# Kernel optimization log

Hardware: AMD Instinct MI355X
Metric: run time of the kernel (lower is better)

## Reference

```python
import jax, jax.numpy as jnp
import numpy as np

B, T, H, DK, DV, HID = 2, 2048, 6, 256, 256, 2048
EPS = 1e-5


def setup_inputs() -> dict:
    key = jax.random.key(0)
    ks = jax.random.split(key, 12)
    sd = 0.02
    hidden_ab = jax.random.normal(ks[0], (B, T, HID), jnp.float32)
    hidden_g = jax.random.normal(ks[1], (B, T, HID), jnp.float32)
    q = jax.random.normal(ks[2], (B, T, H, DK), jnp.float32)
    k = jax.random.normal(ks[3], (B, T, H, DK), jnp.float32)
    v = jax.random.normal(ks[4], (B, T, H, DV), jnp.float32)
    b_w = jax.random.normal(ks[5], (H, HID), jnp.float32) * sd
    a_w = jax.random.normal(ks[6], (H, HID), jnp.float32) * sd
    g_w = jax.random.normal(ks[7], (H, HID), jnp.float32) * sd
    A_log = jnp.log(jax.random.uniform(ks[8], (H,), jnp.float32, 1.0, 16.0))
    dt = jnp.exp(jax.random.uniform(ks[9], (H,), jnp.float32)
                 * (np.log(0.1) - np.log(0.001)) + np.log(0.001))
    dt = jnp.clip(dt, 1e-4)
    dt_bias = dt + jnp.log(-jnp.expm1(-dt))
    norm_w = jnp.ones((DV,), jnp.float32)
    o_w = jax.random.normal(ks[10], (H, DV, DK), jnp.float32) * sd
    return dict(hidden_ab=hidden_ab, hidden_g=hidden_g, q=q, k=k, v=v,
                b_w=b_w, a_w=a_w, A_log=A_log, dt_bias=dt_bias,
                g_w=g_w, norm_w=norm_w, o_w=o_w)


def _l2norm(x):
    return x * jax.lax.rsqrt(jnp.sum(x * x, axis=-1, keepdims=True) + 1e-6)


def _gated_delta_rule(q, k, v, g, beta):
    # q,k: [B,T,H,DK]; v: [B,T,H,DV]; g,beta: [B,T,H]
    q = _l2norm(q) * (DK ** -0.5)
    k = _l2norm(k)
    # time-major for scan
    qT = jnp.swapaxes(q, 0, 1)
    kT = jnp.swapaxes(k, 0, 1)
    vT = jnp.swapaxes(v, 0, 1)
    gT = jnp.swapaxes(g, 0, 1)
    bT = jnp.swapaxes(beta, 0, 1)

    def step(S, xs):
        qt, kt, vt, gt, bt = xs  # [B,H,*]
        S = S * jnp.exp(gt)[..., None, None]            # gated decay
        pred = jnp.einsum('bhk,bhkv->bhv', kt, S)        # current prediction
        delta = (vt - pred) * bt[..., None]              # beta-scaled error
        S = S + jnp.einsum('bhk,bhv->bhkv', kt, delta)   # delta-rule update
        ot = jnp.einsum('bhk,bhkv->bhv', qt, S)
        return S, ot

    S0 = jnp.zeros((B, H, DK, DV), q.dtype)
    _, oT = jax.lax.scan(step, S0, (qT, kT, vT, gT, bT))
    return jnp.swapaxes(oT, 0, 1)  # [B,T,H,DV]


def reference(hidden_ab, hidden_g, q, k, v, b_w, a_w, A_log, dt_bias, g_w, norm_w, o_w):
    beta = jax.nn.sigmoid(jnp.einsum('bth,nh->btn', hidden_ab, b_w))        # [B,T,H]
    g = -jnp.exp(A_log) * jax.nn.softplus(
        jnp.einsum('bth,nh->btn', hidden_ab, a_w) + dt_bias)                 # [B,T,H]
    o = _gated_delta_rule(q, k, v, g, beta)                                  # [B,T,H,DV]
    # FusedRMSNormSwishGate with per-head scalar gate
    gate = jnp.einsum('bth,nh->btn', hidden_g, g_w)                          # [B,T,H]
    o_n = o * jax.lax.rsqrt(jnp.mean(o * o, axis=-1, keepdims=True) + EPS) * norm_w
    o_n = o_n * (gate * jax.nn.sigmoid(gate))[..., None]
    # GroupLinear per head: head_v_dim -> head_dim
    out = jnp.einsum('bthv,hvd->bthd', o_n, o_w).reshape(B, T, H * DK)
    return out
```

## Files before the change

kernel.cpp:

```cpp
#include <hip/hip_runtime.h>
#include <hip/hip_bf16.h>
#include <math.h>

#define B_ 2
#define T_ 2048
#define H_ 6
#define DK_ 256
#define DV_ 256
#define HID_ 2048
#define C_ 64
#define NC_ 32

typedef __attribute__((ext_vector_type(8))) short short8;
typedef __attribute__((ext_vector_type(4))) float f32x4;

__device__ __forceinline__ unsigned rnebf(float f) {
  unsigned u = __float_as_uint(f);
  return (u + 0x7fffu + ((u >> 16) & 1u)) >> 16;
}
__device__ __forceinline__ unsigned pkbf(float lo, float hi) {
  return rnebf(lo) | (rnebf(hi) << 16);
}
__device__ __forceinline__ float bf2f(unsigned u16v) {
  return __uint_as_float((u16v & 0xffffu) << 16);
}
__device__ __forceinline__ short8 u4_to_s8(uint4 u) {
  union { uint4 u; short8 s; } c; c.u = u; return c.s;
}

__device__ __forceinline__ void gload_lds16(const void* g, void* l) {
  __builtin_amdgcn_global_load_lds(
      (const __attribute__((address_space(1))) unsigned int*)g,
      (__attribute__((address_space(3))) unsigned int*)l, 16, 0, 0);
}

__device__ __forceinline__ short8 buildB(uint2 Pe, uint2 Po, int lg, int c16) {
  const int src0 = ((2 * (lg & 1)) << 4) | c16;
  const int src1 = src0 + 16;
  int e0 = __shfl((int)Pe.x, src0), o0 = __shfl((int)Po.x, src0);
  int e1 = __shfl((int)Pe.y, src0), o1 = __shfl((int)Po.y, src0);
  int e2 = __shfl((int)Pe.x, src1), o2 = __shfl((int)Po.x, src1);
  int e3 = __shfl((int)Pe.y, src1), o3 = __shfl((int)Po.y, src1);
  const bool lo2 = (lg < 2);
  union { int i[4]; short8 s; } u;
  u.i[0] = lo2 ? e0 : o0;
  u.i[1] = lo2 ? e1 : o1;
  u.i[2] = lo2 ? e2 : o2;
  u.i[3] = lo2 ? e3 : o3;
  return u.s;
}

__global__ __launch_bounds__(256) void gdn_proj_kernel(
    const float* __restrict__ hab, const float* __restrict__ hg,
    const float* __restrict__ b_w, const float* __restrict__ a_w,
    const float* __restrict__ g_w, const float* __restrict__ A_log,
    const float* __restrict__ dt_bias,
    float* __restrict__ beta_o, float* __restrict__ g_o,
    float* __restrict__ sgate_o) {
  const int bt = blockIdx.x;
  const int tid = threadIdx.x;
  const int lane = tid & 63;
  const int wid = tid >> 6;

  const float* h1 = hab + (size_t)bt * HID_ + tid * 8;
  const float* h2 = hg + (size_t)bt * HID_ + tid * 8;
  const float4 xa = *(const float4*)(h1);
  const float4 xb = *(const float4*)(h1 + 4);
  const float4 ya = *(const float4*)(h2);
  const float4 yb = *(const float4*)(h2 + 4);

  float part[18];
#pragma unroll
  for (int n = 0; n < 6; ++n) {
    const float* wp = b_w + n * HID_ + tid * 8;
    const float4 w0 = *(const float4*)(wp);
    const float4 w1 = *(const float4*)(wp + 4);
    part[n] = xa.x * w0.x + xa.y * w0.y + xa.z * w0.z + xa.w * w0.w +
              xb.x * w1.x + xb.y * w1.y + xb.z * w1.z + xb.w * w1.w;
  }
#pragma unroll
  for (int n = 0; n < 6; ++n) {
    const float* wp = a_w + n * HID_ + tid * 8;
    const float4 w0 = *(const float4*)(wp);
    const float4 w1 = *(const float4*)(wp + 4);
    part[6 + n] = xa.x * w0.x + xa.y * w0.y + xa.z * w0.z + xa.w * w0.w +
                  xb.x * w1.x + xb.y * w1.y + xb.z * w1.z + xb.w * w1.w;
  }
#pragma unroll
  for (int n = 0; n < 6; ++n) {
    const float* wp = g_w + n * HID_ + tid * 8;
    const float4 w0 = *(const float4*)(wp);
    const float4 w1 = *(const float4*)(wp + 4);
    part[12 + n] = ya.x * w0.x + ya.y * w0.y + ya.z * w0.z + ya.w * w0.w +
                   yb.x * w1.x + yb.y * w1.y + yb.z * w1.z + yb.w * w1.w;
  }

  __shared__ float red[18][4];
#pragma unroll
  for (int i = 0; i < 18; ++i) {
    float x = part[i];
    x += __shfl_xor(x, 1);
    x += __shfl_xor(x, 2);
    x += __shfl_xor(x, 4);
    x += __shfl_xor(x, 8);
    x += __shfl_xor(x, 16);
    x += __shfl_xor(x, 32);
    if (lane == 0) red[i][wid] = x;
  }
  __syncthreads();

  if (tid < 18) {
    const float s = red[tid][0] + red[tid][1] + red[tid][2] + red[tid][3];
    if (tid < 6) {
      beta_o[(size_t)bt * H_ + tid] = 1.f / (1.f + __expf(-s));
    } else if (tid < 12) {
      const int n = tid - 6;
      const float x = s + dt_bias[n];
      const float sp = (x > 20.f) ? x : log1pf(__expf(x));
      g_o[(size_t)bt * H_ + n] = -__expf(A_log[n]) * sp;
    } else {
      const int n = tid - 12;
      sgate_o[(size_t)bt * H_ + n] = s / (1.f + __expf(-s));
    }
  }
}

__global__ __launch_bounds__(256) void gdn_cum_kernel(
    const float* __restrict__ g, float* __restrict__ Gc,
    float* __restrict__ lam) {
  const int bh = blockIdx.x;
  const int b = bh / H_, h = bh - b * H_;
  const int w = threadIdx.x >> 6, l = threadIdx.x & 63;
  for (int it = 0; it < 8; ++it) {
    const int nc = it * 4 + w;
    const int tg = nc * C_ + l;
    const size_t srow = ((size_t)b * T_ + tg) * H_ + h;
    float val = g[srow];
#pragma unroll
    for (int ofs = 1; ofs < 64; ofs <<= 1) {
      const float o = __shfl_up(val, ofs);
      if (l >= ofs) val += o;
    }
    Gc[(bh * NC_ + nc) * C_ + l] = val;
    if (l == 63) lam[bh * NC_ + nc] = __expf(val);
  }
}

__global__ __launch_bounds__(256) void gdn_prep_mfma_kernel(
    const float* __restrict__ q, const float* __restrict__ k,
    const float* __restrict__ beta, const float* __restrict__ Gc,
    ushort* __restrict__ wWp, ushort* __restrict__ wMp,
    ushort* __restrict__ wQd, ushort* __restrict__ wkT,
    float* __restrict__ wAlT, float* __restrict__ wScl,
    const float* __restrict__ o_w, ushort* __restrict__ owT) {
  __shared__ __attribute__((aligned(16))) char smem[77312];

  const int bid = blockIdx.x;
  const int tid = threadIdx.x;

  if (bid >= 512) {
    const int b2 = bid - 512;
    const int h2 = b2 >> 2;
    const int db = (b2 & 3) * 64;
    ushort* t = (ushort*)smem;
#pragma unroll
    for (int it = 0; it < 16; ++it) {
      const int v2 = it * 16 + (tid >> 4);
      const int dl = 4 * (tid & 15);
      const float4 x =
          *(const float4*)&o_w[((size_t)h2 * 256 + v2) * 256 + db + dl];
      t[(dl + 0) * 264 + v2] = (ushort)rnebf(x.x);
      t[(dl + 1) * 264 + v2] = (ushort)rnebf(x.y);
      t[(dl + 2) * 264 + v2] = (ushort)rnebf(x.z);
      t[(dl + 3) * 264 + v2] = (ushort)rnebf(x.w);
    }
    __syncthreads();
#pragma unroll
    for (int it = 0; it < 8; ++it) {
      const int idx = it * 256 + tid;
      const int d = idx >> 5;
      const int vv = (idx & 31) * 8;
      uint4 o;
      o.x = *(uint*)&t[d * 264 + vv + 0]; o.y = *(uint*)&t[d * 264 + vv + 2];
      o.z = *(uint*)&t[d * 264 + vv + 4]; o.w = *(uint*)&t[d * 264 + vv + 6];
      *(uint4*)&owT[((size_t)h2 * 256 + db + d) * 256 + vv] = o;
    }
    return;
  }

  const int bhx = bid & 15;
  if (bhx >= B_ * H_) return;
  const int nc = bid >> 4;
  const int bh = bhx;
  const int b = bh / H_, h = bh - b * H_;
  const int w = tid >> 6, l = tid & 63;
  const int lg = l >> 4, c16 = l & 15;
  const int cidx = bh * NC_ + nc;

  ushort* knB = (ushort*)smem;
  ushort* qnB = (ushort*)(smem + 32768);
  ushort* Msc = (ushort*)(smem + 65536);
  float* bG = (float*)(smem + 74752);
  float* bB = bG + 64;
  float* bSc = bG + 128;
  float* bWl = bG + 192;
  float* bKg = bG + 256;
  float* bQg = bG + 320;
  float* bSk = bG + 384;
  float* bSq = bG + 448;
  float* bQe = bG + 512;

  const size_t srow0 = ((size_t)b * T_ + nc * C_) * H_ + h;
  if (tid < C_) {
    bG[tid] = Gc[cidx * C_ + tid];
    bB[tid] = beta[srow0 + (size_t)tid * H_];
  }
  __syncthreads();

#pragma unroll
  for (int rr = 0; rr < 16; ++rr) {
    const int row = rr * 4 + w;
    const size_t g0 = (srow0 + (size_t)row * H_) * DK_;
    const float4 kv = *(const float4*)(k + g0 + 4 * l);
    const float4 qv = *(const float4*)(q + g0 + 4 * l);
    const int boff = row * 512 + ((8 * l) ^ ((row & 7) << 4));
    uint2 pk_, pq_;
    pk_.x = pkbf(kv.x, kv.y); pk_.y = pkbf(kv.z, kv.w);
    pq_.x = pkbf(qv.x, qv.y); pq_.y = pkbf(qv.z, qv.w);
    *(uint2*)((char*)knB + boff) = pk_;
    *(uint2*)((char*)qnB + boff) = pq_;
  }
  __syncthreads();

  f32x4 accm[4], acca[4];
  {
    const int xorv = (c16 & 7) << 4;
    const int rowA = 16 * w + c16;
    uint4 aq[8], ak[8];
#pragma unroll
    for (int kt = 0; kt < 8; ++kt) {
      const int coff = (64 * kt + 16 * lg) ^ xorv;
      aq[kt] = *(const uint4*)((char*)qnB + rowA * 512 + coff);
      ak[kt] = *(const uint4*)((char*)knB + rowA * 512 + coff);
    }
#pragma unroll
    for (int nt = 0; nt < 4; ++nt) {
      accm[nt] = (f32x4){0.f, 0.f, 0.f, 0.f};
      acca[nt] = (f32x4){0.f, 0.f, 0.f, 0.f};
    }
    f32x4 accq = (f32x4){0.f, 0.f, 0.f, 0.f};
#pragma unroll
    for (int nt = 0; nt < 4; ++nt) {
      const int rowB = 16 * nt + c16;
#pragma unroll
      for (int kt = 0; kt < 8; ++kt) {
        const uint4 bk =
            *(const uint4*)((char*)knB + rowB * 512 + ((64 * kt + 16 * lg) ^ xorv));
        const short8 bkf = u4_to_s8(bk);
        accm[nt] = __builtin_amdgcn_mfma_f32_16x16x32_bf16(u4_to_s8(aq[kt]),
                                                           bkf, accm[nt], 0, 0, 0);
        acca[nt] = __builtin_amdgcn_mfma_f32_16x16x32_bf16(u4_to_s8(ak[kt]),
                                                           bkf, acca[nt], 0, 0, 0);
      }
    }
#pragma unroll
    for (int kt = 0; kt < 8; ++kt) {
      const short8 bq = u4_to_s8(aq[kt]);
      accq = __builtin_amdgcn_mfma_f32_16x16x32_bf16(bq, bq, accq, 0, 0, 0);
    }
#pragma unroll
    for (int r = 0; r < 4; ++r) {
      if ((c16 >> 2) == lg && (c16 & 3) == r) {
        bKg[16 * w + c16] = acca[w][r];
        bQg[16 * w + c16] = accq[r];
      }
    }
  }
  __syncthreads();

  if (tid < C_) {
    const float gv = bG[tid];
    const float gend = bG[C_ - 1];
    const float skv = rsqrtf(bKg[tid] + 1e-6f);
    const float sqv = rsqrtf(bQg[tid] + 1e-6f) * 0.0625f;
    bSk[tid] = skv;
    bSq[tid] = sqv;
    bSc[tid] = __expf(gend - gv) * skv;
    bWl[tid] = bB[tid] * __expf(gv) * skv;
    bQe[tid] = sqv * __expf(gv);
  }
  __syncthreads();

  {
    float* gA = wAlT + (size_t)cidx * 4096;
#pragma unroll
    for (int nt = 0; nt < 4; ++nt) {
#pragma unroll
      for (int r = 0; r < 4; ++r) {
        const int t = 16 * w + 4 * lg + r;
        const int i = 16 * nt + c16;
        const float eg = __expf(bG[t] - bG[i]);
        const float ski = bSk[i];
        Msc[t * 72 + i] =
            (ushort)((i <= t) ? rnebf(accm[nt][r] * bSq[t] * ski * eg) : 0u);
        gA[i * 64 + t] =
            (i < t) ? bB[t] * bSk[t] * ski * eg * acca[nt][r] : 0.f;
      }
    }
  }
  {
    const int d = tid;
    ushort* wb = wWp + (size_t)cidx * C_ * 256;
#pragma unroll
    for (int e = 0; e < 8; ++e) {
      float vj[8];
#pragma unroll
      for (int j = 0; j < 8; ++j) {
        const int t = 8 * e + j;
        const float kv = bf2f(*(const ushort*)((char*)knB + t * 512 +
                                               ((2 * d) ^ ((t & 7) << 4))));
        vj[j] = kv;
        wb[t * 256 + d] = (ushort)rnebf(kv * bWl[t]);
      }
      uint4 o;
      o.x = pkbf(vj[0] * bSc[8 * e + 0], vj[1] * bSc[8 * e + 1]);
      o.y = pkbf(vj[2] * bSc[8 * e + 2], vj[3] * bSc[8 * e + 3]);
      o.z = pkbf(vj[4] * bSc[8 * e + 4], vj[5] * bSc[8 * e + 5]);
      o.w = pkbf(vj[6] * bSc[8 * e + 6], vj[7] * bSc[8 * e + 7]);
      *(uint4*)&wkT[((size_t)cidx * 256 + d) * C_ + 8 * e] = o;
    }
  }
#pragma unroll
  for (int rr = 0; rr < 16; ++rr) {
    const int row = rr * 4 + w;
    const float qe = bQe[row];
    const uint2 pq =
        *(const uint2*)((char*)qnB + row * 512 + ((8 * l) ^ ((row & 7) << 4)));
    const float q0 = bf2f(pq.x), q1 = bf2f(pq.x >> 16);
    const float q2 = bf2f(pq.y), q3 = bf2f(pq.y >> 16);
    uint2 oq;
    oq.x = pkbf(q0 * qe, q1 * qe);
    oq.y = pkbf(q2 * qe, q3 * qe);
    *(uint2*)&wQd[(srow0 + (size_t)row * H_) * DK_ + 4 * l] = oq;
  }
  __syncthreads();

  {
    const int row = tid >> 2;
#pragma unroll
    for (int e = 0; e < 2; ++e) {
      const int col = ((tid & 3) * 2 + e) * 8;
      *(uint4*)&wMp[(size_t)cidx * C_ * C_ + row * C_ + col] =
          *(const uint4*)&Msc[row * 72 + col];
    }
  }
  (void)wScl;
}

__global__ __launch_bounds__(256) void gdn_prep_fs_kernel(
    const float* __restrict__ v, const float* __restrict__ beta,
    const float* __restrict__ wAlT, ushort* __restrict__ wWp,
    uint2* __restrict__ wUp) {
  __shared__ __attribute__((aligned(16))) float AlT[64 * 68];
  __shared__ float bB[64];

  const int slot = blockIdx.x;
  const int bhx = slot & 15;
  if (bhx >= B_ * H_) return;
  const int nc = slot >> 4;
  const int bh = bhx;
  const int b = bh / H_, h = bh - b * H_;
  const int tid = threadIdx.x;
  const int cidx = bh * NC_ + nc;
  const size_t srow0 = ((size_t)b * T_ + nc * C_) * H_ + h;

  {
    const float* gA = wAlT + (size_t)cidx * 4096;
#pragma unroll
    for (int it = 0; it < 16; ++it) {
      const int idx = it * 256 + tid;
      AlT[(idx >> 6) * 68 + (idx & 63)] = gA[idx];
    }
  }
  if (tid < C_) bB[tid] = beta[srow0 + (size_t)tid * H_];
  __syncthreads();

  float xw[64];
  ushort* wb = wWp + (size_t)cidx * C_ * 256;
#pragma unroll
  for (int t = 0; t < C_; ++t) xw[t] = bf2f(wb[t * 256 + tid]);

  float xu[64];
#pragma unroll
  for (int t = 0; t < C_; ++t)
    xu[t] = v[(srow0 + (size_t)t * H_) * DV_ + tid] * bB[t];

#pragma unroll
  for (int tb = 0; tb < 8; ++tb) {
#pragma unroll
    for (int i = 0; i < 8 * tb; ++i) {
      const float xui = xu[i];
      const float xwi = xw[i];
      float av[8];
      *(float4*)&av[0] = *(float4*)&AlT[i * 68 + 8 * tb];
      *(float4*)&av[4] = *(float4*)&AlT[i * 68 + 8 * tb + 4];
#pragma unroll
      for (int e = 0; e < 8; ++e) {
        xu[8 * tb + e] = fmaf(-av[e], xui, xu[8 * tb + e]);
        xw[8 * tb + e] = fmaf(-av[e], xwi, xw[8 * tb + e]);
      }
    }
#pragma unroll
    for (int e = 1; e < 8; ++e)
#pragma unroll
      for (int m = 0; m < 7; ++m)
        if (m < e) {
          const float am = AlT[(8 * tb + m) * 68 + 8 * tb + e];
          xu[8 * tb + e] = fmaf(-am, xu[8 * tb + m], xu[8 * tb + e]);
          xw[8 * tb + e] = fmaf(-am, xw[8 * tb + m], xw[8 * tb + e]);
        }
  }
  {
#pragma unroll
    for (int row = 0; row < C_; ++row)
      wb[row * 256 + tid] = (ushort)rnebf(xw[row]);
    const int cbw = tid >> 4, c16s = tid & 15;
#pragma unroll
    for (int mt = 0; mt < 4; ++mt) {
#pragma unroll
      for (int lgi = 0; lgi < 4; ++lgi) {
        const int r0 = 16 * mt + 4 * lgi;
        uint2 val;
        val.x = pkbf(xu[r0 + 0], xu[r0 + 1]);
        val.y = pkbf(xu[r0 + 2], xu[r0 + 3]);
        wUp[(((size_t)cidx * 16 + cbw) * 4 + mt) * 64 + (lgi << 4) + c16s] = val;
      }
    }
  }
}

__global__ __launch_bounds__(128, 1) void gdn_seq_kernel(
    const ushort* __restrict__ wkT, const ushort* __restrict__ wWp,
    const uint2* __restrict__ wUp, const float* __restrict__ lam,
    uint2* __restrict__ wDP, uint2* __restrict__ wSP) {
  const int bid = blockIdx.x;
  const int cb = bid >> 4, bhx = bid & 15;
  if (bhx >= B_ * H_) return;
  const int bh = bhx;
  const int tid = threadIdx.x;
  const int kh = tid >> 6, l = tid & 63;
  const int lg = l >> 4, c16 = l & 15;
  const int xorv = (c16 & 7) << 4;

  __shared__ ushort sW[2][16384];
  __shared__ ushort sK[2][16384];
  __shared__ uint2 sU[2][256];
  __shared__ f32x4 sX[2][4][64];
  __shared__ float sLam[NC_];

  auto stage = [&](int pp, int cidx2) {
    const char* gw_ = (const char*)(wWp + (size_t)cidx2 * 16384);
#pragma unroll
    for (int j = 0; j < 16; ++j) {
      const int i = kh * 16 + j;
      const int row = 2 * i + (l >> 5);
      const int colb = ((l & 31) * 16) ^ ((row & 7) << 4);
      gload_lds16(gw_ + row * 512 + colb, (char*)&sW[pp][0] + i * 1024);
    }
    const char* gk_ = (const char*)(wkT + (size_t)cidx2 * 16384);
#pragma unroll
    for (int j = 0; j < 16; ++j) {
      const int i = kh * 16 + j;
      const int row = 8 * i + (l >> 3);
      const int colb = ((l & 7) * 16) ^ ((row & 7) << 4);
      gload_lds16(gk_ + row * 128 + colb, (char*)&sK[pp][0] + i * 1024);
    }
    const char* gu_ = (const char*)wUp + ((size_t)cidx2 * 16 + cb) * 2048;
    gload_lds16(gu_ + kh * 1024 + l * 16, (char*)&sU[pp][0] + kh * 1024);
  };

  f32x4 S[8];
#pragma unroll
  for (int m2 = 0; m2 < 8; ++m2) S[m2] = (f32x4){0.f, 0.f, 0.f, 0.f};

  stage(0, bh * NC_ + 0);
  stage(1, bh * NC_ + 1);
  if (tid < NC_) sLam[tid] = lam[bh * NC_ + tid];
  asm volatile("s_waitcnt lgkmcnt(0)" ::: "memory");
  __builtin_amdgcn_sched_barrier(0);
  __builtin_amdgcn_s_barrier();
  __builtin_amdgcn_sched_barrier(0);

  for (int nc = 0; nc < NC_; ++nc) {
    const int pp = nc & 1;
    const int cidx = bh * NC_ + nc;
    if (nc == 0)
      asm volatile("s_waitcnt vmcnt(33)" ::: "memory");
    else if (nc == NC_ - 1)
      asm volatile("s_waitcnt vmcnt(5)" ::: "memory");
    else
      asm volatile("s_waitcnt vmcnt(38)" ::: "memory");
    __builtin_amdgcn_sched_barrier(0);
    __builtin_amdgcn_s_barrier();
    __builtin_amdgcn_sched_barrier(0);

    uint2 P[8];
#pragma unroll
    for (int m2 = 0; m2 < 8; ++m2) {
      P[m2].x = pkbf(S[m2][0], S[m2][1]);
      P[m2].y = pkbf(S[m2][2], S[m2][3]);
    }
    {
      uint4* sp4 = (uint4*)(wSP + (((size_t)cidx * 16 + cb) * 64 + l) * 16 +
                            kh * 8);
#pragma unroll
      for (int i = 0; i < 4; ++i) {
        uint4 o; o.x = P[2 * i].x; o.y = P[2 * i].y;
        o.z = P[2 * i + 1].x; o.w = P[2 * i + 1].y;
        sp4[i] = o;
      }
    }

    f32x4 pe[4], po[4];
#pragma unroll
    for (int mt = 0; mt < 4; ++mt) {
      pe[mt] = (f32x4){0.f, 0.f, 0.f, 0.f};
      po[mt] = (f32x4){0.f, 0.f, 0.f, 0.f};
    }
    const char* sWb = (const char*)&sW[pp][0];
#pragma unroll
    for (int ktl = 0; ktl < 4; ++ktl) {
      const int kt = kh * 4 + ktl;
      const short8 Bf = buildB(P[2 * ktl], P[2 * ktl + 1], lg, c16);
      const int colb = (64 * kt + 16 * lg) ^ xorv;
#pragma unroll
      for (int mt = 0; mt < 4; ++mt) {
        const uint4 aw = *(const uint4*)(sWb + (16 * mt + c16) * 512 + colb);
        if (ktl & 1)
          po[mt] = __builtin_amdgcn_mfma_f32_16x16x32_bf16(u4_to_s8(aw), Bf,
                                                           po[mt], 0, 0, 0);
        else
          pe[mt] = __builtin_amdgcn_mfma_f32_16x16x32_bf16(u4_to_s8(aw), Bf,
                                                           pe[mt], 0, 0, 0);
      }
    }
    f32x4 pl[4];
#pragma unroll
    for (int mt = 0; mt < 4; ++mt) {
      pl[mt] = pe[mt] + po[mt];
      sX[kh][mt][l] = pl[mt];
    }
    asm volatile("s_waitcnt lgkmcnt(0)" ::: "memory");
    __builtin_amdgcn_sched_barrier(0);
    __builtin_amdgcn_s_barrier();
    __builtin_amdgcn_sched_barrier(0);

    uint2 DP[4];
#pragma unroll
    for (int mt = 0; mt < 4; ++mt) {
      const f32x4 pr = sX[kh ^ 1][mt][l];
      const uint2 uu = sU[pp][mt * 64 + l];
      const float d0 = bf2f(uu.x) - (pl[mt][0] + pr[0]);
      const float d1 = bf2f(uu.x >> 16) - (pl[mt][1] + pr[1]);
      const float d2 = bf2f(uu.y) - (pl[mt][2] + pr[2]);
      const float d3 = bf2f(uu.y >> 16) - (pl[mt][3] + pr[3]);
      DP[mt].x = pkbf(d0, d1);
      DP[mt].y = pkbf(d2, d3);
    }
    {
      uint4* dp4 = (uint4*)(wDP + (((size_t)cidx * 16 + cb) * 64 + l) * 4);
      uint4 od;
      if (kh == 0) { od.x = DP[0].x; od.y = DP[0].y; od.z = DP[1].x; od.w = DP[1].y; }
      else         { od.x = DP[2].x; od.y = DP[2].y; od.z = DP[3].x; od.w = DP[3].y; }
      dp4[kh] = od;
    }
    const float lamC = sLam[nc];
#pragma unroll
    for (int m2 = 0; m2 < 8; ++m2) {
      S[m2][0] *= lamC; S[m2][1] *= lamC; S[m2][2] *= lamC; S[m2][3] *= lamC;
    }
    const char* sKb = (const char*)&sK[pp][0];
#pragma unroll
    for (int kt2 = 0; kt2 < 2; ++kt2) {
      const short8 Bd = buildB(DP[2 * kt2], DP[2 * kt2 + 1], lg, c16);
      const int colb = (64 * kt2 + 16 * lg) ^ xorv;
#pragma unroll
      for (int m2 = 0; m2 < 8; ++m2) {
        const int m2g = kh * 8 + m2;
        const uint4 ak = *(const uint4*)(sKb + (16 * m2g + c16) * 128 + colb);
        S[m2] = __builtin_amdgcn_mfma_f32_16x16x32_bf16(u4_to_s8(ak), Bd,
                                                        S[m2], 0, 0, 0);
      }
    }
    __builtin_amdgcn_sched_barrier(0);
    __builtin_amdgcn_s_barrier();
    __builtin_amdgcn_sched_barrier(0);
    if (nc + 2 < NC_) stage(pp, cidx + 2);
    __builtin_amdgcn_sched_barrier(0);
  }
}

__global__ __launch_bounds__(256) void gdn_ofin_kernel(
    const ushort* __restrict__ wQd, const ushort* __restrict__ wMp,
    const uint2* __restrict__ wDP, const uint2* __restrict__ wSP,
    const float* __restrict__ sgate, const float* __restrict__ norm_w,
    const ushort* __restrict__ owT, float* __restrict__ out) {
  const int slot = blockIdx.x;
  const int bhx = slot & 15;
  if (bhx >= B_ * H_) return;
  const int nc = slot >> 4;
  const int bh = bhx;
  const int cidx = bh * NC_ + nc;
  const int b = bh / H_, h = bh - b * H_;
  const int tid = threadIdx.x;
  const int w = tid >> 6, l = tid & 63;
  const int lg = l >> 4, c16 = l & 15;
  const size_t t0 = (size_t)b * T_ + nc * C_;

  __shared__ ushort onl[64 * 256];
  __shared__ float red[64][4];
  __shared__ float rowf[64];

  f32x4 acc[4][4];
#pragma unroll
  for (int mt = 0; mt < 4; ++mt)
#pragma unroll
    for (int nt = 0; nt < 4; ++nt) acc[mt][nt] = (f32x4){0.f, 0.f, 0.f, 0.f};

#pragma unroll
  for (int nt = 0; nt < 4; ++nt) {
    const int cbwq = 4 * w + nt;
    uint2 SPl[16];
    const uint4* sp4 =
        (const uint4*)(wSP + (((size_t)cidx * 16 + cbwq) * 64 + l) * 16);
#pragma unroll
    for (int i = 0; i < 8; ++i) {
      const uint4 t4 = sp4[i];
      SPl[2 * i].x = t4.x; SPl[2 * i].y = t4.y;
      SPl[2 * i + 1].x = t4.z; SPl[2 * i + 1].y = t4.w;
    }
#pragma unroll
    for (int kt = 0; kt < 8; ++kt) {
      const short8 Bf = buildB(SPl[2 * kt], SPl[2 * kt + 1], lg, c16);
#pragma unroll
      for (int mt = 0; mt < 4; ++mt) {
        const uint4 aq = *(const uint4*)&wQd[((t0 + 16 * mt + c16) * H_ + h) *
                                                 (size_t)DK_ +
                                             32 * kt + 8 * lg];
        acc[mt][nt] = __builtin_amdgcn_mfma_f32_16x16x32_bf16(
            u4_to_s8(aq), Bf, acc[mt][nt], 0, 0, 0);
      }
    }
  }
  const ushort* Mb = wMp + (size_t)cidx * C_ * C_;
#pragma unroll
  for (int nt = 0; nt < 4; ++nt) {
    const int cbwq = 4 * w + nt;
    uint2 DPl[4];
    {
      const uint4* dp4 =
          (const uint4*)(wDP + (((size_t)cidx * 16 + cbwq) * 64 + l) * 4);
      const uint4 a0 = dp4[0], a1 = dp4[1];
      DPl[0].x = a0.x; DPl[0].y = a0.y; DPl[1].x = a0.z; DPl[1].y = a0.w;
      DPl[2].x = a1.x; DPl[2].y = a1.y; DPl[3].x = a1.z; DPl[3].y = a1.w;
    }
#pragma unroll
    for (int kt2 = 0; kt2 < 2; ++kt2) {
      const short8 Bf = buildB(DPl[2 * kt2], DPl[2 * kt2 + 1], lg, c16);
#pragma unroll
      for (int mt = 0; mt < 4; ++mt) {
        const uint4 am =
            *(const uint4*)&Mb[(16 * mt + c16) * C_ + 32 * kt2 + 8 * lg];
        acc[mt][nt] = __builtin_amdgcn_mfma_f32_16x16x32_bf16(
            u4_to_s8(am), Bf, acc[mt][nt], 0, 0, 0);
      }
    }
  }

  float ss[4][4];
#pragma unroll
  for (int mt = 0; mt < 4; ++mt)
#pragma unroll
    for (int r = 0; r < 4; ++r) {
      float s = acc[mt][0][r] * acc[mt][0][r];
      s = fmaf(acc[mt][1][r], acc[mt][1][r], s);
      s = fmaf(acc[mt][2][r], acc[mt][2][r], s);
      s = fmaf(acc[mt][3][r], acc[mt][3][r], s);
      s += __shfl_xor(s, 1);
      s += __shfl_xor(s, 2);
      s += __shfl_xor(s, 4);
      s += __shfl_xor(s, 8);
      ss[mt][r] = s;
    }
  if (c16 == 0) {
#pragma unroll
    for (int mt = 0; mt < 4; ++mt)
#pragma unroll
      for (int r = 0; r < 4; ++r) red[16 * mt + 4 * lg + r][w] = ss[mt][r];
  }
  __syncthreads();
  if (tid < 64) {
    const float ms =
        (red[tid][0] + red[tid][1] + red[tid][2] + red[tid][3]) * (1.f / DV_);
    const float sg = sgate[(t0 + tid) * H_ + h];
    rowf[tid] = rsqrtf(ms + 1e-5f) * sg;
  }
  __syncthreads();

  {
    char* onb = (char*)onl;
#pragma unroll
    for (int mt = 0; mt < 4; ++mt) {
      float rf[4];
#pragma unroll
      for (int r = 0; r < 4; ++r) rf[r] = rowf[16 * mt + 4 * lg + r];
#pragma unroll
      for (int nt = 0; nt < 4; ++nt) {
        const int c = (4 * w + nt) * 16 + c16;
        const float nwv = norm_w[c];
#pragma unroll
        for (int r = 0; r < 4; ++r) {
          const int row = 16 * mt + 4 * lg + r;
          const float v = acc[mt][nt][r] * rf[r] * nwv;
          *(ushort*)(onb + row * 512 + ((2 * c) ^ ((row & 7) << 4))) =
              (ushort)rnebf(v);
        }
      }
    }
  }
  __syncthreads();

  f32x4 acc2[4][4];
#pragma unroll
  for (int mt = 0; mt < 4; ++mt)
#pragma unroll
    for (int nt2 = 0; nt2 < 4; ++nt2)
      acc2[mt][nt2] = (f32x4){0.f, 0.f, 0.f, 0.f};
  {
    const char* onb = (const char*)onl;
#pragma unroll
    for (int kt = 0; kt < 8; ++kt) {
      uint4 af[4];
#pragma unroll
      for (int mt = 0; mt < 4; ++mt)
        af[mt] = *(const uint4*)(onb + (16 * mt + c16) * 512 +
                                 ((64 * kt + 16 * lg) ^ ((c16 & 7) << 4)));
#pragma unroll
      for (int nt2 = 0; nt2 < 4; ++nt2) {
        const uint4 bf = *(const uint4*)&owT[((size_t)h * 256 +
                                              (4 * w + nt2) * 16 + c16) *
                                                 256 +
                                             32 * kt + 8 * lg];
#pragma unroll
        for (int mt = 0; mt < 4; ++mt)
          acc2[mt][nt2] = __builtin_amdgcn_mfma_f32_16x16x32_bf16(
              u4_to_s8(af[mt]), u4_to_s8(bf), acc2[mt][nt2], 0, 0, 0);
      }
    }
  }
#pragma unroll
  for (int mt = 0; mt < 4; ++mt)
#pragma unroll
    for (int nt2 = 0; nt2 < 4; ++nt2)
#pragma unroll
      for (int r = 0; r < 4; ++r)
        out[((t0 + 16 * mt + 4 * lg + r) * H_ + h) * (size_t)DK_ +
            (4 * w + nt2) * 16 + c16] = acc2[mt][nt2][r];
}

extern "C" void kernel_launch(void* const* d_in, const int* in_sizes, int n_in,
                              void* d_out, int out_size, void* d_ws,
                              size_t ws_size, hipStream_t stream) {
  const float* hab = (const float*)d_in[0];
  const float* hg = (const float*)d_in[1];
  const float* q = (const float*)d_in[2];
  const float* k = (const float*)d_in[3];
  const float* v = (const float*)d_in[4];
  const float* b_w = (const float*)d_in[5];
  const float* a_w = (const float*)d_in[6];
  const float* A_log = (const float*)d_in[7];
  const float* dt_bias = (const float*)d_in[8];
  const float* g_w = (const float*)d_in[9];
  const float* norm_w = (const float*)d_in[10];
  const float* o_w = (const float*)d_in[11];
  float* out = (float*)d_out;

  float* ws = (float*)d_ws;
  const size_t NBT = (size_t)B_ * T_ * H_;
  float* w_beta = ws;
  float* w_g = ws + NBT;
  float* w_sg = ws + 2 * NBT;
  float* w_G = ws + 5 * NBT;
  float* w_lam = ws + 7 * NBT;
  ushort* w_Qd = (ushort*)(ws + 7 * NBT + 1024);
  ushort* w_kT = w_Qd + (size_t)12582912;
  ushort* w_W = w_kT + (size_t)6291456;
  ushort* w_M = w_W + (size_t)6291456;
  uint2* w_U = (uint2*)(w_M + (size_t)1572864);
  uint2* w_DP = w_U + (size_t)1572864;
  uint2* w_SP = w_DP + (size_t)1572864;
  ushort* w_owT = (ushort*)(w_SP + (size_t)6291456);
  float* w_AlT = (float*)(w_owT + (size_t)393216);

  hipLaunchKernelGGL(gdn_proj_kernel, dim3(B_ * T_), dim3(256), 0, stream,
                     hab, hg, b_w, a_w, g_w, A_log, dt_bias, w_beta, w_g,
                     w_sg);
  hipLaunchKernelGGL(gdn_cum_kernel, dim3(B_ * H_), dim3(256), 0, stream,
                     w_g, w_G, w_lam);
  hipLaunchKernelGGL(gdn_prep_mfma_kernel, dim3(512 + 24), dim3(256), 0,
                     stream, q, k, w_beta, w_G, w_W, w_M, w_Qd, w_kT, w_AlT,
                     nullptr, o_w, w_owT);
  hipLaunchKernelGGL(gdn_prep_fs_kernel, dim3(512), dim3(256), 0, stream,
                     v, w_beta, w_AlT, w_W, w_U);
  hipLaunchKernelGGL(gdn_seq_kernel, dim3(256), dim3(128), 0, stream,
                     w_kT, w_W, w_U, w_lam, w_DP, w_SP);
  hipLaunchKernelGGL(gdn_ofin_kernel, dim3(512), dim3(256), 0, stream,
                     w_Qd, w_M, w_DP, w_SP, w_sg, norm_w, w_owT, out);
}
```

Measured before the change: 250.7 us.

## Split sequential chunk-state kernel across four waves instead of two

The sequential inter-chunk state kernel now runs with 256 threads (four wavefronts) per block instead of 128. Each wave holds a quarter of the state tile and a quarter of the K-reduction for the prediction. Partial predictions are combined through a larger shared buffer with a four-way sum, and staging loads plus the waitcnt thresholds are rescaled to match. The aim is to shorten the serial per-chunk critical path by spreading MFMA work over more SIMDs, at the cost of more cross-wave reduction traffic and duplicated delta computation and stores.

Measured after the change: 268.4 us. +7.1%, slower.

```diff
diff --git a/kernel.cpp b/kernel.cpp
--- a/kernel.cpp
+++ b/kernel.cpp
@@ -439,7 +439,7 @@
   }
 }
 
-__global__ __launch_bounds__(128, 1) void gdn_seq_kernel(
+__global__ __launch_bounds__(256, 1) void gdn_seq_kernel(
     const ushort* __restrict__ wkT, const ushort* __restrict__ wWp,
     const uint2* __restrict__ wUp, const float* __restrict__ lam,
     uint2* __restrict__ wDP, uint2* __restrict__ wSP) {
@@ -455,33 +455,34 @@
   __shared__ ushort sW[2][16384];
   __shared__ ushort sK[2][16384];
   __shared__ uint2 sU[2][256];
-  __shared__ f32x4 sX[2][4][64];
+  __shared__ f32x4 sX[4][4][64];
   __shared__ float sLam[NC_];
 
   auto stage = [&](int pp, int cidx2) {
     const char* gw_ = (const char*)(wWp + (size_t)cidx2 * 16384);
 #pragma unroll
-    for (int j = 0; j < 16; ++j) {
-      const int i = kh * 16 + j;
+    for (int j = 0; j < 8; ++j) {
+      const int i = kh * 8 + j;
       const int row = 2 * i + (l >> 5);
       const int colb = ((l & 31) * 16) ^ ((row & 7) << 4);
       gload_lds16(gw_ + row * 512 + colb, (char*)&sW[pp][0] + i * 1024);
     }
     const char* gk_ = (const char*)(wkT + (size_t)cidx2 * 16384);
 #pragma unroll
-    for (int j = 0; j < 16; ++j) {
-      const int i = kh * 16 + j;
+    for (int j = 0; j < 8; ++j) {
+      const int i = kh * 8 + j;
       const int row = 8 * i + (l >> 3);
       const int colb = ((l & 7) * 16) ^ ((row & 7) << 4);
       gload_lds16(gk_ + row * 128 + colb, (char*)&sK[pp][0] + i * 1024);
     }
     const char* gu_ = (const char*)wUp + ((size_t)cidx2 * 16 + cb) * 2048;
-    gload_lds16(gu_ + kh * 1024 + l * 16, (char*)&sU[pp][0] + kh * 1024);
+    const int iu = kh & 1;
+    gload_lds16(gu_ + iu * 1024 + l * 16, (char*)&sU[pp][0] + iu * 1024);
   };
 
-  f32x4 S[8];
-#pragma unroll
-  for (int m2 = 0; m2 < 8; ++m2) S[m2] = (f32x4){0.f, 0.f, 0.f, 0.f};
+  f32x4 S[4];
+#pragma unroll
+  for (int m2 = 0; m2 < 4; ++m2) S[m2] = (f32x4){0.f, 0.f, 0.f, 0.f};
 
   stage(0, bh * NC_ + 0);
   stage(1, bh * NC_ + 1);
@@ -495,30 +496,27 @@
     const int pp = nc & 1;
     const int cidx = bh * NC_ + nc;
     if (nc == 0)
-      asm volatile("s_waitcnt vmcnt(33)" ::: "memory");
+      asm volatile("s_waitcnt vmcnt(17)" ::: "memory");
     else if (nc == NC_ - 1)
-      asm volatile("s_waitcnt vmcnt(5)" ::: "memory");
+      asm volatile("s_waitcnt vmcnt(3)" ::: "memory");
     else
-      asm volatile("s_waitcnt vmcnt(38)" ::: "memory");
+      asm volatile("s_waitcnt vmcnt(20)" ::: "memory");
     __builtin_amdgcn_sched_barrier(0);
     __builtin_amdgcn_s_barrier();
     __builtin_amdgcn_sched_barrier(0);
 
-    uint2 P[8];
-#pragma unroll
-    for (int m2 = 0; m2 < 8; ++m2) {
+    uint2 P[4];
+#pragma unroll
+    for (int m2 = 0; m2 < 4; ++m2) {
       P[m2].x = pkbf(S[m2][0], S[m2][1]);
       P[m2].y = pkbf(S[m2][2], S[m2][3]);
     }
     {
       uint4* sp4 = (uint4*)(wSP + (((size_t)cidx * 16 + cb) * 64 + l) * 16 +
-                            kh * 8);
-#pragma unroll
-      for (int i = 0; i < 4; ++i) {
-        uint4 o; o.x = P[2 * i].x; o.y = P[2 * i].y;
-        o.z = P[2 * i + 1].x; o.w = P[2 * i + 1].y;
-        sp4[i] = o;
-      }
+                            kh * 4);
+      uint4 o0; o0.x = P[0].x; o0.y = P[0].y; o0.z = P[1].x; o0.w = P[1].y;
+      uint4 o1; o1.x = P[2].x; o1.y = P[2].y; o1.z = P[3].x; o1.w = P[3].y;
+      sp4[0] = o0; sp4[1] = o1;
     }
 
     f32x4 pe[4], po[4];
@@ -529,8 +527,8 @@
     }
     const char* sWb = (const char*)&sW[pp][0];
 #pragma unroll
-    for (int ktl = 0; ktl < 4; ++ktl) {
-      const int kt = kh * 4 + ktl;
+    for (int ktl = 0; ktl < 2; ++ktl) {
+      const int kt = kh * 2 + ktl;
       const short8 Bf = buildB(P[2 * ktl], P[2 * ktl + 1], lg, c16);
       const int colb = (64 * kt + 16 * lg) ^ xorv;
 #pragma unroll
@@ -544,12 +542,8 @@
                                                            pe[mt], 0, 0, 0);
       }
     }
-    f32x4 pl[4];
-#pragma unroll
-    for (int mt = 0; mt < 4; ++mt) {
-      pl[mt] = pe[mt] + po[mt];
-      sX[kh][mt][l] = pl[mt];
-    }
+#pragma unroll
+    for (int mt = 0; mt < 4; ++mt) sX[kh][mt][l] = pe[mt] + po[mt];
     asm volatile("s_waitcnt lgkmcnt(0)" ::: "memory");
     __builtin_amdgcn_sched_barrier(0);
     __builtin_amdgcn_s_barrier();
@@ -558,25 +552,28 @@
     uint2 DP[4];
 #pragma unroll
     for (int mt = 0; mt < 4; ++mt) {
-      const f32x4 pr = sX[kh ^ 1][mt][l];
+      const f32x4 p0 = sX[0][mt][l];
+      const f32x4 p1 = sX[1][mt][l];
+      const f32x4 p2 = sX[2][mt][l];
+      const f32x4 p3 = sX[3][mt][l];
       const uint2 uu = sU[pp][mt * 64 + l];
-      const float d0 = bf2f(uu.x) - (pl[mt][0] + pr[0]);
-      const float d1 = bf2f(uu.x >> 16) - (pl[mt][1] + pr[1]);
-      const float d2 = bf2f(uu.y) - (pl[mt][2] + pr[2]);
-      const float d3 = bf2f(uu.y >> 16) - (pl[mt][3] + pr[3]);
+      const float d0 = bf2f(uu.x) - ((p0[0] + p1[0]) + (p2[0] + p3[0]));
+      const float d1 = bf2f(uu.x >> 16) - ((p0[1] + p1[1]) + (p2[1] + p3[1]));
+      const float d2 = bf2f(uu.y) - ((p0[2] + p1[2]) + (p2[2] + p3[2]));
+      const float d3 = bf2f(uu.y >> 16) - ((p0[3] + p1[3]) + (p2[3] + p3[3]));
       DP[mt].x = pkbf(d0, d1);
       DP[mt].y = pkbf(d2, d3);
     }
     {
       uint4* dp4 = (uint4*)(wDP + (((size_t)cidx * 16 + cb) * 64 + l) * 4);
       uint4 od;
-      if (kh == 0) { od.x = DP[0].x; od.y = DP[0].y; od.z = DP[1].x; od.w = DP[1].y; }
-      else         { od.x = DP[2].x; od.y = DP[2].y; od.z = DP[3].x; od.w = DP[3].y; }
-      dp4[kh] = od;
+      if ((kh & 1) == 0) { od.x = DP[0].x; od.y = DP[0].y; od.z = DP[1].x; od.w = DP[1].y; }
+      else               { od.x = DP[2].x; od.y = DP[2].y; od.z = DP[3].x; od.w = DP[3].y; }
+      dp4[kh & 1] = od;
     }
     const float lamC = sLam[nc];
 #pragma unroll
-    for (int m2 = 0; m2 < 8; ++m2) {
+    for (int m2 = 0; m2 < 4; ++m2) {
       S[m2][0] *= lamC; S[m2][1] *= lamC; S[m2][2] *= lamC; S[m2][3] *= lamC;
     }
     const char* sKb = (const char*)&sK[pp][0];
@@ -585,8 +582,8 @@
       const short8 Bd = buildB(DP[2 * kt2], DP[2 * kt2 + 1], lg, c16);
       const int colb = (64 * kt2 + 16 * lg) ^ xorv;
 #pragma unroll
-      for (int m2 = 0; m2 < 8; ++m2) {
-        const int m2g = kh * 8 + m2;
+      for (int m2 = 0; m2 < 4; ++m2) {
+        const int m2g = kh * 4 + m2;
         const uint4 ak = *(const uint4*)(sKb + (16 * m2g + c16) * 128 + colb);
         S[m2] = __builtin_amdgcn_mfma_f32_16x16x32_bf16(u4_to_s8(ak), Bd,
                                                         S[m2], 0, 0, 0);
@@ -812,7 +809,7 @@
                      nullptr, o_w, w_owT);
   hipLaunchKernelGGL(gdn_prep_fs_kernel, dim3(512), dim3(256), 0, stream,
                      v, w_beta, w_AlT, w_W, w_U);
-  hipLaunchKernelGGL(gdn_seq_kernel, dim3(256), dim3(128), 0, stream,
+  hipLaunchKernelGGL(gdn_seq_kernel, dim3(256), dim3(256), 0, stream,
                      w_kT, w_W, w_U, w_lam, w_DP, w_SP);
   hipLaunchKernelGGL(gdn_ofin_kernel, dim3(512), dim3(256), 0, stream,
                      w_Qd, w_M, w_DP, w_SP, w_sg, norm_w, w_owT, out);
```
